# Kernel optimization log

Hardware: AMD Instinct MI355X
Metric: run time of the kernel (lower is better)

Reference implementation:

```python
import jax, jax.numpy as jnp
import numpy as np

N_NODES = 50000
N_EDGES = 1000000
NUM_FEATURES = 32
EDGE_DIM = 16
H = 64
L = 2
BN_EPS = 1e-5
GIN_EPS = 0.0


def _lin(k, fan_in, fan_out, scale=0.1):
    kw, kb = jax.random.split(k)
    W = jax.random.normal(kw, (fan_in, fan_out), jnp.float32) * scale
    b = jax.random.normal(kb, (fan_out,), jnp.float32) * scale
    return W, b


def setup_inputs() -> dict:
    key = jax.random.key(0)
    ks = jax.random.split(key, 12)
    x = jax.random.normal(ks[0], (N_NODES, NUM_FEATURES), jnp.float32)
    edge_index = jax.random.randint(ks[1], (2, N_EDGES), 0, N_NODES, jnp.int64 if jax.config.read('jax_enable_x64') else jnp.int32)
    edge_attr = jax.random.normal(ks[2], (N_EDGES, EDGE_DIM), jnp.float32)
    node_W, node_b = _lin(ks[3], NUM_FEATURES, H)
    edge_W, edge_b = _lin(ks[4], EDGE_DIM, H)

    def stack_lin(k, fan_in, fan_out):
        Ws, bs = zip(*[_lin(kk, fan_in, fan_out) for kk in jax.random.split(k, L)])
        return jnp.stack(Ws), jnp.stack(bs)

    elin_W, elin_b = stack_lin(ks[5], H, H)      # GINEConv internal edge lin
    mlp1_W, mlp1_b = stack_lin(ks[6], H, H)      # GINEConv nn layer 1
    mlp2_W, mlp2_b = stack_lin(ks[7], H, H)      # GINEConv nn layer 2
    emlp1_W, emlp1_b = stack_lin(ks[8], 3 * H, H)  # edge-update MLP layer 1
    emlp2_W, emlp2_b = stack_lin(ks[9], H, H)      # edge-update MLP layer 2
    bn_gamma = jnp.ones((L, H), jnp.float32)
    bn_beta = jnp.zeros((L, H), jnp.float32)
    return dict(x=x, edge_index=edge_index, edge_attr=edge_attr,
                node_W=node_W, node_b=node_b, edge_W=edge_W, edge_b=edge_b,
                elin_W=elin_W, elin_b=elin_b,
                mlp1_W=mlp1_W, mlp1_b=mlp1_b, mlp2_W=mlp2_W, mlp2_b=mlp2_b,
                emlp1_W=emlp1_W, emlp1_b=emlp1_b, emlp2_W=emlp2_W, emlp2_b=emlp2_b,
                bn_gamma=bn_gamma, bn_beta=bn_beta)


def reference(x, edge_index, edge_attr,
              node_W, node_b, edge_W, edge_b,
              elin_W, elin_b, mlp1_W, mlp1_b, mlp2_W, mlp2_b,
              emlp1_W, emlp1_b, emlp2_W, emlp2_b, bn_gamma, bn_beta):
    src, dst = edge_index[0], edge_index[1]
    n = x.shape[0]
    h = x @ node_W + node_b                     # [N, H]
    ea = edge_attr @ edge_W + edge_b            # [E, H]
    for i in range(L):
        # GINEConv: message = relu(x_src + lin(edge_attr)), sum-aggregate at dst
        msg = jax.nn.relu(h[src] + ea @ elin_W[i] + elin_b[i])        # [E, H]
        agg = jax.ops.segment_sum(msg, dst, num_segments=n)           # [N, H]
        out = (1.0 + GIN_EPS) * h + agg
        out = jax.nn.relu(out @ mlp1_W[i] + mlp1_b[i]) @ mlp2_W[i] + mlp2_b[i]
        # BatchNorm (training-mode batch statistics, biased variance)
        mu = out.mean(axis=0)
        var = out.var(axis=0)
        out = (out - mu) * jax.lax.rsqrt(var + BN_EPS) * bn_gamma[i] + bn_beta[i]
        h = (h + jax.nn.relu(out)) * 0.5
        # edge update: gather-concat-MLP residual
        e_in = jnp.concatenate([h[src], h[dst], ea], axis=-1)         # [E, 3H]
        e_up = jax.nn.relu(e_in @ emlp1_W[i] + emlp1_b[i]) @ emlp2_W[i] + emlp2_b[i]
        ea = ea + e_up * 0.5
    return h, ea
```

## Files before the change

### kernel.cpp

```cpp
#include <hip/hip_runtime.h>
#include <hip/hip_bf16.h>

#define NN 50000
#define NE 1000000
#define NF 32
#define ED 16
#define HD 64
#define BN_EPS 1e-5f

typedef unsigned short u16;
typedef __attribute__((ext_vector_type(8))) short bf16x8;
typedef __attribute__((ext_vector_type(4))) float f32x4;

#define WAVE_SYNC() do { \
    asm volatile("s_waitcnt lgkmcnt(0)" ::: "memory"); \
    __builtin_amdgcn_sched_barrier(0); \
} while (0)

__device__ __forceinline__ u16 f2b(float x)
{
    __hip_bfloat16 b = __float2bfloat16(x);
    u16 u; __builtin_memcpy(&u, &b, 2); return u;
}
__device__ __forceinline__ float b2f(u16 u)
{
    uint v = (uint)u << 16; float f; __builtin_memcpy(&f, &v, 4); return f;
}

__global__ __launch_bounds__(256) void k_fill(float* p, float v, size_t n)
{
    size_t i = (size_t)blockIdx.x * 256 + threadIdx.x;
    if (i < n) p[i] = v;
}

__device__ __forceinline__ void gemm4(float (&o)[HD], float4 t, const float* __restrict__ Wr)
{
    #pragma unroll
    for (int f = 0; f < HD; f++) o[f] = fmaf(t.x, Wr[f], o[f]);
    #pragma unroll
    for (int f = 0; f < HD; f++) o[f] = fmaf(t.y, Wr[HD + f], o[f]);
    #pragma unroll
    for (int f = 0; f < HD; f++) o[f] = fmaf(t.z, Wr[2 * HD + f], o[f]);
    #pragma unroll
    for (int f = 0; f < HD; f++) o[f] = fmaf(t.w, Wr[3 * HD + f], o[f]);
}

__global__ __launch_bounds__(256) void k_prep_w1(const float* __restrict__ W, u16* __restrict__ out)
{
    int idx = blockIdx.x * 256 + threadIdx.x;
    if (idx >= 2 * 192 * HD) return;
    int l = idx / (192 * HD), r = idx % (192 * HD), k = r / HD, f = r % HD;
    out[l * 192 * HD + f * 192 + k] = f2b(W[idx]);
}
__global__ __launch_bounds__(256) void k_prep_w64(const float* __restrict__ W, u16* __restrict__ out)
{
    int idx = blockIdx.x * 256 + threadIdx.x;
    if (idx >= 2 * HD * HD) return;
    int l = idx / (HD * HD), r = idx % (HD * HD), k = r / HD, f = r % HD;
    out[l * HD * HD + f * HD + k] = f2b(W[idx]);
}

__global__ __launch_bounds__(256) void k_node_proj(
    const float* __restrict__ x, const float* __restrict__ W,
    const float* __restrict__ b, float* __restrict__ h)
{
    __shared__ float sW[NF * HD];
    for (int t = threadIdx.x; t < NF * HD; t += 256) sW[t] = W[t];
    __syncthreads();
    int lane = threadIdx.x & 63, wv = threadIdx.x >> 6;
    int n = blockIdx.x * 4 + wv;
    if (n >= NN) return;
    float a = (lane < NF) ? x[(size_t)n * NF + lane] : 0.f;
    float acc = b[lane];
    #pragma unroll
    for (int k = 0; k < NF; k++) acc = fmaf(__shfl(a, k), sW[k * HD + lane], acc);
    h[(size_t)n * HD + lane] = acc;
}

__global__ __launch_bounds__(256) void k_edge_proj(
    const float* __restrict__ attr, const float* __restrict__ W,
    const float* __restrict__ b, u16* __restrict__ eab)
{
    size_t e = (size_t)blockIdx.x * 256 + threadIdx.x;
    if (e >= NE) return;
    float o[HD];
    #pragma unroll
    for (int f = 0; f < HD; f++) o[f] = b[f];
    const float4* ar = (const float4*)(attr + e * ED);
    #pragma unroll
    for (int k4 = 0; k4 < ED / 4; k4++)
        gemm4(o, ar[k4], W + (k4 * 4) * HD);
    uint* er = (uint*)(eab + e * HD);
    #pragma unroll
    for (int f2 = 0; f2 < 32; f2++)
        er[f2] = (uint)f2b(o[2 * f2]) | ((uint)f2b(o[2 * f2 + 1]) << 16);
}

__global__ __launch_bounds__(256) void k_gine_msg_mfma(
    const u16* __restrict__ eab, const float* __restrict__ h,
    const int* __restrict__ src, const int* __restrict__ dst,
    const u16* __restrict__ wt, const float* __restrict__ b,
    float* __restrict__ agg)
{
    const int lane = threadIdx.x & 63, wv = threadIdx.x >> 6;
    const size_t base = ((size_t)blockIdx.x * 4 + wv) * 32;
    if (base >= NE) return;
    const int c = lane & 15, g = lane >> 4;

    bf16x8 ae[2][2];
    #pragma unroll
    for (int s = 0; s < 2; s++) {
        const u16* ep = &eab[(base + 16 * s + c) * HD + 8 * g];
        ae[s][0] = *(const bf16x8*)ep;
        ae[s][1] = *(const bf16x8*)(ep + 32);
    }
    int sv[2][4], dv[2][4];
    #pragma unroll
    for (int s = 0; s < 2; s++)
        #pragma unroll
        for (int r = 0; r < 4; r++) {
            sv[s][r] = src[base + 16 * s + 4 * g + r];
            dv[s][r] = dst[base + 16 * s + 4 * g + r];
        }

    f32x4 acc[2][4];
    #pragma unroll
    for (int s = 0; s < 2; s++)
        #pragma unroll
        for (int tt = 0; tt < 4; tt++) {
            float bv = b[tt * 16 + c];
            acc[s][tt] = (f32x4){bv, bv, bv, bv};
        }
    #pragma unroll
    for (int ki = 0; ki < 2; ki++)
        #pragma unroll
        for (int tt = 0; tt < 4; tt++) {
            bf16x8 bw = *(const bf16x8*)&wt[(tt * 16 + c) * HD + ki * 32 + 8 * g];
            acc[0][tt] = __builtin_amdgcn_mfma_f32_16x16x32_bf16(ae[0][ki], bw, acc[0][tt], 0, 0, 0);
            acc[1][tt] = __builtin_amdgcn_mfma_f32_16x16x32_bf16(ae[1][ki], bw, acc[1][tt], 0, 0, 0);
        }
    #pragma unroll
    for (int s = 0; s < 2; s++)
        #pragma unroll
        for (int tt = 0; tt < 4; tt++)
            #pragma unroll
            for (int r = 0; r < 4; r++) {
                float m = acc[s][tt][r] + h[(size_t)sv[s][r] * HD + tt * 16 + c];
                m = fmaxf(m, 0.f);
                unsafeAtomicAdd(&agg[(size_t)dv[s][r] * HD + tt * 16 + c], m);
            }
}

__global__ __launch_bounds__(256) void k_node_mlp(
    const float* __restrict__ h, const float* __restrict__ agg,
    const float* __restrict__ W1, const float* __restrict__ b1,
    const float* __restrict__ W2, const float* __restrict__ b2,
    float* __restrict__ out2)
{
    int n = blockIdx.x * 256 + threadIdx.x;
    if (n >= NN) return;
    float o[HD];
    #pragma unroll
    for (int f = 0; f < HD; f++) o[f] = b1[f];
    const float4* hr = (const float4*)(h + (size_t)n * HD);
    const float4* ar = (const float4*)(agg + (size_t)n * HD);
    #pragma unroll 4
    for (int k4 = 0; k4 < 16; k4++) {
        float4 t1 = hr[k4], t2 = ar[k4];
        float4 t = make_float4(t1.x + t2.x, t1.y + t2.y, t1.z + t2.z, t1.w + t2.w);
        gemm4(o, t, W1 + (k4 * 4) * HD);
    }
    #pragma unroll
    for (int k = 0; k < HD; k++) o[k] = fmaxf(o[k], 0.f);
    #pragma unroll
    for (int c = 0; c < 4; c++) {
        float p[16];
        #pragma unroll
        for (int j = 0; j < 16; j++) p[j] = b2[c * 16 + j];
        for (int k = 0; k < HD; k++) {
            const float* Wr = W2 + k * HD + c * 16;
            #pragma unroll
            for (int j = 0; j < 16; j++) p[j] = fmaf(o[k], Wr[j], p[j]);
        }
        float4* orow = (float4*)(out2 + (size_t)n * HD + c * 16);
        #pragma unroll
        for (int q = 0; q < 4; q++)
            orow[q] = make_float4(p[4*q], p[4*q+1], p[4*q+2], p[4*q+3]);
    }
}

__global__ __launch_bounds__(256) void k_bnstats(
    const float* __restrict__ out2, float* __restrict__ bnst)
{
    int f = threadIdx.x & 63;
    int row0 = blockIdx.x * 4 + (threadIdx.x >> 6);
    float s = 0.f, q = 0.f;
    for (int r = row0; r < NN; r += gridDim.x * 4) {
        float v = out2[(size_t)r * HD + f];
        s += v; q += v * v;
    }
    unsafeAtomicAdd(&bnst[f], s);
    unsafeAtomicAdd(&bnst[HD + f], q);
}

__global__ __launch_bounds__(256) void k_bn_h(
    const float* __restrict__ out2, const float* __restrict__ bnst,
    const float* __restrict__ gamma, const float* __restrict__ beta,
    float* __restrict__ h, u16* __restrict__ hbf, float* __restrict__ hout, int last)
{
    size_t idx = (size_t)blockIdx.x * 256 + threadIdx.x;
    if (idx >= (size_t)NN * HD) return;
    int f = (int)(idx & 63);
    float mu  = bnst[f] * (1.f / NN);
    float var = bnst[HD + f] * (1.f / NN) - mu * mu;
    float sc  = gamma[f] * rsqrtf(var + BN_EPS);
    float sh  = beta[f] - mu * sc;
    float o   = fmaxf(fmaf(out2[idx], sc, sh), 0.f);
    float hn  = (h[idx] + o) * 0.5f;
    h[idx] = hn;
    hbf[idx] = f2b(hn);
    if (last) hout[idx] = hn;
}

__device__ __forceinline__ void edge_mlp_core(
    const u16* __restrict__ hbf, const u16* __restrict__ eab,
    const int* __restrict__ src, const int* __restrict__ dst,
    const u16* __restrict__ w1t, const float* __restrict__ b1,
    const u16* __restrict__ w2t, const float* __restrict__ b2,
    u16* sOw, size_t base, int c, int g, f32x4 (&acc2)[2][4])
{
    int sv[2], dv[2];
    #pragma unroll
    for (int s = 0; s < 2; s++) {
        sv[s] = src[base + 16 * s + c];
        dv[s] = dst[base + 16 * s + c];
    }
    bf16x8 A[3][2][2];
    #pragma unroll
    for (int s = 0; s < 2; s++) {
        const u16* hs = &hbf[(size_t)sv[s] * HD + 8 * g];
        A[0][s][0] = *(const bf16x8*)hs;
        A[0][s][1] = *(const bf16x8*)(hs + 32);
        const u16* hd = &hbf[(size_t)dv[s] * HD + 8 * g];
        A[1][s][0] = *(const bf16x8*)hd;
        A[1][s][1] = *(const bf16x8*)(hd + 32);
        const u16* ep = &eab[(base + 16 * s + c) * HD + 8 * g];
        A[2][s][0] = *(const bf16x8*)ep;
        A[2][s][1] = *(const bf16x8*)(ep + 32);
    }
    f32x4 acc[2][4];
    #pragma unroll
    for (int s = 0; s < 2; s++)
        #pragma unroll
        for (int tt = 0; tt < 4; tt++) {
            float bv = b1[tt * 16 + c];
            acc[s][tt] = (f32x4){bv, bv, bv, bv};
        }
    #pragma unroll
    for (int sec = 0; sec < 3; sec++)
        #pragma unroll
        for (int ki = 0; ki < 2; ki++)
            #pragma unroll
            for (int tt = 0; tt < 4; tt++) {
                bf16x8 bw = *(const bf16x8*)&w1t[(tt * 16 + c) * 192 + sec * 64 + ki * 32 + 8 * g];
                acc[0][tt] = __builtin_amdgcn_mfma_f32_16x16x32_bf16(A[sec][0][ki], bw, acc[0][tt], 0, 0, 0);
                acc[1][tt] = __builtin_amdgcn_mfma_f32_16x16x32_bf16(A[sec][1][ki], bw, acc[1][tt], 0, 0, 0);
            }
    #pragma unroll
    for (int s = 0; s < 2; s++)
        #pragma unroll
        for (int tt = 0; tt < 4; tt++)
            #pragma unroll
            for (int r = 0; r < 4; r++)
                sOw[(16 * s + 4 * g + r) * 72 + tt * 16 + c] = f2b(fmaxf(acc[s][tt][r], 0.f));
    WAVE_SYNC();
    bf16x8 A2[2][2];
    #pragma unroll
    for (int s = 0; s < 2; s++) {
        A2[s][0] = *(const bf16x8*)&sOw[(16 * s + c) * 72 + 8 * g];
        A2[s][1] = *(const bf16x8*)&sOw[(16 * s + c) * 72 + 32 + 8 * g];
    }
    WAVE_SYNC();
    #pragma unroll
    for (int s = 0; s < 2; s++)
        #pragma unroll
        for (int tt = 0; tt < 4; tt++) {
            float bv = b2[tt * 16 + c];
            acc2[s][tt] = (f32x4){bv, bv, bv, bv};
        }
    #pragma unroll
    for (int ki = 0; ki < 2; ki++)
        #pragma unroll
        for (int tt = 0; tt < 4; tt++) {
            bf16x8 bw = *(const bf16x8*)&w2t[(tt * 16 + c) * HD + ki * 32 + 8 * g];
            acc2[0][tt] = __builtin_amdgcn_mfma_f32_16x16x32_bf16(A2[0][ki], bw, acc2[0][tt], 0, 0, 0);
            acc2[1][tt] = __builtin_amdgcn_mfma_f32_16x16x32_bf16(A2[1][ki], bw, acc2[1][tt], 0, 0, 0);
        }
}

__global__ __launch_bounds__(256) void k_edge_upd_fused(
    const u16* __restrict__ hbf, u16* __restrict__ eab,
    const int* __restrict__ src, const int* __restrict__ dst,
    const u16* __restrict__ w1t, const float* __restrict__ b1,
    const u16* __restrict__ w2t, const float* __restrict__ b2,
    const float* __restrict__ h, const u16* __restrict__ welt,
    const float* __restrict__ belin, float* __restrict__ agg)
{
    __shared__ u16 sO[4][32 * 72];
    const int lane = threadIdx.x & 63, wv = threadIdx.x >> 6;
    const size_t base = ((size_t)blockIdx.x * 4 + wv) * 32;
    if (base >= NE) return;
    u16* sOw = sO[wv];
    const int c = lane & 15, g = lane >> 4;

    f32x4 acc2[2][4];
    edge_mlp_core(hbf, eab, src, dst, w1t, b1, w2t, b2, sOw, base, c, g, acc2);

    #pragma unroll
    for (int s = 0; s < 2; s++)
        #pragma unroll
        for (int tt = 0; tt < 4; tt++)
            #pragma unroll
            for (int r = 0; r < 4; r++) {
                size_t a = (base + 16 * s + 4 * g + r) * HD + tt * 16 + c;
                u16 nb = f2b(b2f(eab[a]) + 0.5f * acc2[s][tt][r]);
                eab[a] = nb;
                sOw[(16 * s + 4 * g + r) * 72 + tt * 16 + c] = nb;
            }
    WAVE_SYNC();

    bf16x8 A3[2][2];
    #pragma unroll
    for (int s = 0; s < 2; s++) {
        A3[s][0] = *(const bf16x8*)&sOw[(16 * s + c) * 72 + 8 * g];
        A3[s][1] = *(const bf16x8*)&sOw[(16 * s + c) * 72 + 32 + 8 * g];
    }
    f32x4 acc3[2][4];
    #pragma unroll
    for (int s = 0; s < 2; s++)
        #pragma unroll
        for (int tt = 0; tt < 4; tt++) {
            float bv = belin[tt * 16 + c];
            acc3[s][tt] = (f32x4){bv, bv, bv, bv};
        }
    #pragma unroll
    for (int ki = 0; ki < 2; ki++)
        #pragma unroll
        for (int tt = 0; tt < 4; tt++) {
            bf16x8 bw = *(const bf16x8*)&welt[(tt * 16 + c) * HD + ki * 32 + 8 * g];
            acc3[0][tt] = __builtin_amdgcn_mfma_f32_16x16x32_bf16(A3[0][ki], bw, acc3[0][tt], 0, 0, 0);
            acc3[1][tt] = __builtin_amdgcn_mfma_f32_16x16x32_bf16(A3[1][ki], bw, acc3[1][tt], 0, 0, 0);
        }
    int sv2[2][4], dv2[2][4];
    #pragma unroll
    for (int s = 0; s < 2; s++)
        #pragma unroll
        for (int r = 0; r < 4; r++) {
            sv2[s][r] = src[base + 16 * s + 4 * g + r];
            dv2[s][r] = dst[base + 16 * s + 4 * g + r];
        }
    #pragma unroll
    for (int s = 0; s < 2; s++)
        #pragma unroll
        for (int tt = 0; tt < 4; tt++)
            #pragma unroll
            for (int r = 0; r < 4; r++) {
                float m = acc3[s][tt][r] + h[(size_t)sv2[s][r] * HD + tt * 16 + c];
                m = fmaxf(m, 0.f);
                unsafeAtomicAdd(&agg[(size_t)dv2[s][r] * HD + tt * 16 + c], m);
            }
}

__global__ __launch_bounds__(256) void k_edge_upd_final(
    const u16* __restrict__ hbf, const u16* __restrict__ eab,
    float* __restrict__ eaout,
    const int* __restrict__ src, const int* __restrict__ dst,
    const u16* __restrict__ w1t, const float* __restrict__ b1,
    const u16* __restrict__ w2t, const float* __restrict__ b2)
{
    __shared__ u16 sO[4][32 * 72];
    const int lane = threadIdx.x & 63, wv = threadIdx.x >> 6;
    const size_t base = ((size_t)blockIdx.x * 4 + wv) * 32;
    if (base >= NE) return;
    u16* sOw = sO[wv];
    const int c = lane & 15, g = lane >> 4;

    f32x4 acc2[2][4];
    edge_mlp_core(hbf, eab, src, dst, w1t, b1, w2t, b2, sOw, base, c, g, acc2);

    #pragma unroll
    for (int s = 0; s < 2; s++)
        #pragma unroll
        for (int tt = 0; tt < 4; tt++)
            #pragma unroll
            for (int r = 0; r < 4; r++) {
                size_t a = (base + 16 * s + 4 * g + r) * HD + tt * 16 + c;
                eaout[a] = b2f(eab[a]) + 0.5f * acc2[s][tt][r];
            }
}

extern "C" void kernel_launch(void* const* d_in, const int* in_sizes, int n_in,
                              void* d_out, int out_size, void* d_ws, size_t ws_size,
                              hipStream_t stream)
{
    const float* x        = (const float*)d_in[0];
    const int*   ei       = (const int*)d_in[1];
    const float* eattr    = (const float*)d_in[2];
    const float* node_W   = (const float*)d_in[3];
    const float* node_b   = (const float*)d_in[4];
    const float* edge_W   = (const float*)d_in[5];
    const float* edge_b   = (const float*)d_in[6];
    const float* elin_W   = (const float*)d_in[7];
    const float* elin_b   = (const float*)d_in[8];
    const float* mlp1_W   = (const float*)d_in[9];
    const float* mlp1_b   = (const float*)d_in[10];
    const float* mlp2_W   = (const float*)d_in[11];
    const float* mlp2_b   = (const float*)d_in[12];
    const float* emlp1_W  = (const float*)d_in[13];
    const float* emlp1_b  = (const float*)d_in[14];
    const float* emlp2_W  = (const float*)d_in[15];
    const float* emlp2_b  = (const float*)d_in[16];
    const float* bn_gamma = (const float*)d_in[17];
    const float* bn_beta  = (const float*)d_in[18];

    float* hout = (float*)d_out;
    float* eaout = hout + (size_t)NN * HD;

    const int* src = ei;
    const int* dst = ei + NE;

    float* hbuf = (float*)d_ws;
    float* agg  = hbuf + (size_t)NN * HD;
    float* out2 = agg + (size_t)NN * HD;
    float* bnst = out2 + (size_t)NN * HD;
    u16*   w1t  = (u16*)(bnst + 128);
    u16*   w2t  = w1t + 2 * 192 * HD;
    u16*   welt = w2t + 2 * HD * HD;
    u16*   hbf  = welt + 2 * HD * HD;
    u16*   eab  = hbf + (size_t)NN * HD;
    size_t base_need = ((size_t)NN * HD * 3 + 128) * sizeof(float)
                     + (2 * 192 * HD + 4 * HD * HD + (size_t)NN * HD
                        + (size_t)NE * HD) * sizeof(u16);

    static const int exp_sizes[19] = {
        1600000, 2000000, 16000000, 2048, 64, 1024, 64,
        8192, 128, 8192, 128, 8192, 128, 24576, 128, 8192, 128, 128, 128};
    float sentinel = 0.f;
    if (n_in != 19) sentinel = 6000.f;
    else {
        for (int i = 0; i < 19; i++)
            if (in_sizes[i] != exp_sizes[i]) { sentinel = 2000.f + 32.f * i; break; }
    }
    if (sentinel == 0.f && ws_size < base_need) sentinel = 7000.f;
    if (sentinel != 0.f) {
        k_fill<<<dim3((unsigned)(((size_t)NN * HD + 255) / 256)), dim3(256), 0, stream>>>(
            hout, sentinel, (size_t)NN * HD);
        k_fill<<<dim3((unsigned)(((size_t)NE * HD + 255) / 256)), dim3(256), 0, stream>>>(
            eaout, 0.f, (size_t)NE * HD);
        return;
    }

    dim3 b256(256);
    const unsigned EG  = (NE + 255) / 256;
    const unsigned WG2 = (NE + 127) / 128;
    k_prep_w1<<<dim3((2 * 192 * HD + 255) / 256), b256, 0, stream>>>(emlp1_W, w1t);
    k_prep_w64<<<dim3((2 * HD * HD + 255) / 256), b256, 0, stream>>>(emlp2_W, w2t);
    k_prep_w64<<<dim3((2 * HD * HD + 255) / 256), b256, 0, stream>>>(elin_W, welt);
    k_node_proj<<<dim3((NN + 3) / 4), b256, 0, stream>>>(x, node_W, node_b, hbuf);
    k_edge_proj<<<dim3(EG), b256, 0, stream>>>(eattr, edge_W, edge_b, eab);

    hipMemsetAsync(agg, 0, (size_t)NN * HD * sizeof(float), stream);
    hipMemsetAsync(bnst, 0, 128 * sizeof(float), stream);
    k_gine_msg_mfma<<<dim3(WG2), b256, 0, stream>>>(
        eab, hbuf, src, dst, welt, elin_b, agg);
    k_node_mlp<<<dim3((NN + 255) / 256), b256, 0, stream>>>(
        hbuf, agg, mlp1_W, mlp1_b, mlp2_W, mlp2_b, out2);
    k_bnstats<<<dim3(256), b256, 0, stream>>>(out2, bnst);
    k_bn_h<<<dim3((NN * HD + 255) / 256), b256, 0, stream>>>(
        out2, bnst, bn_gamma, bn_beta, hbuf, hbf, hout, 0);
    hipMemsetAsync(agg, 0, (size_t)NN * HD * sizeof(float), stream);
    hipMemsetAsync(bnst, 0, 128 * sizeof(float), stream);
    k_edge_upd_fused<<<dim3(WG2), b256, 0, stream>>>(
        hbf, eab, src, dst, w1t, emlp1_b, w2t, emlp2_b,
        hbuf, welt + (size_t)HD * HD, elin_b + HD, agg);

    k_node_mlp<<<dim3((NN + 255) / 256), b256, 0, stream>>>(
        hbuf, agg, mlp1_W + HD * HD, mlp1_b + HD,
        mlp2_W + HD * HD, mlp2_b + HD, out2);
    k_bnstats<<<dim3(256), b256, 0, stream>>>(out2, bnst);
    k_bn_h<<<dim3((NN * HD + 255) / 256), b256, 0, stream>>>(
        out2, bnst, bn_gamma + HD, bn_beta + HD, hbuf, hbf, hout, 1);
    k_edge_upd_final<<<dim3(WG2), b256, 0, stream>>>(
        hbf, eab, eaout, src, dst,
        w1t + (size_t)192 * HD, emlp1_b + HD,
        w2t + (size_t)HD * HD, emlp2_b + HD);
}
```

Baseline: 1.063 ms.

## Fuse edge projection into GINE message kernel via MFMA and prefetch gathers

Replaces the scalar per-thread edge projection kernel with an MFMA projection (edge_W zero-padded to K=32 in bf16) fused into the layer-0 GINE message kernel. The projected edge features are written once and reused from LDS for the elin GEMM, so the bf16 edge array is no longer re-read from global memory. In the fused edge update kernels, the src/dst indices, h gathers and old edge values are loaded up front so their latency overlaps the MLP. This raises register pressure, and edge_attr now passes through bf16 before the projection, which lowers its precision.

```diff
diff --git a/kernel.cpp b/kernel.cpp
--- a/kernel.cpp
+++ b/kernel.cpp
@@ -45,6 +45,18 @@
     for (int f = 0; f < HD; f++) o[f] = fmaf(t.w, Wr[3 * HD + f], o[f]);
 }
 
+__device__ __forceinline__ bf16x8 pack8(const float* __restrict__ p)
+{
+    float4 v0 = ((const float4*)p)[0];
+    float4 v1 = ((const float4*)p)[1];
+    union { uint u[4]; bf16x8 v; } r;
+    r.u[0] = (uint)f2b(v0.x) | ((uint)f2b(v0.y) << 16);
+    r.u[1] = (uint)f2b(v0.z) | ((uint)f2b(v0.w) << 16);
+    r.u[2] = (uint)f2b(v1.x) | ((uint)f2b(v1.y) << 16);
+    r.u[3] = (uint)f2b(v1.z) | ((uint)f2b(v1.w) << 16);
+    return r.v;
+}
+
 __global__ __launch_bounds__(256) void k_prep_w1(const float* __restrict__ W, u16* __restrict__ out)
 {
     int idx = blockIdx.x * 256 + threadIdx.x;
@@ -58,6 +70,13 @@
     if (idx >= 2 * HD * HD) return;
     int l = idx / (HD * HD), r = idx % (HD * HD), k = r / HD, f = r % HD;
     out[l * HD * HD + f * HD + k] = f2b(W[idx]);
+}
+__global__ __launch_bounds__(256) void k_prep_wpad(const float* __restrict__ W, u16* __restrict__ out)
+{
+    int idx = blockIdx.x * 256 + threadIdx.x;
+    if (idx >= HD * 32) return;
+    int f = idx / 32, k = idx % 32;
+    out[f * 32 + k] = (k < ED) ? f2b(W[k * HD + f]) : (u16)0;
 }
 
 __global__ __launch_bounds__(256) void k_node_proj(
@@ -77,67 +96,90 @@
     h[(size_t)n * HD + lane] = acc;
 }
 
-__global__ __launch_bounds__(256) void k_edge_proj(
-    const float* __restrict__ attr, const float* __restrict__ W,
-    const float* __restrict__ b, u16* __restrict__ eab)
-{
-    size_t e = (size_t)blockIdx.x * 256 + threadIdx.x;
-    if (e >= NE) return;
-    float o[HD];
-    #pragma unroll
-    for (int f = 0; f < HD; f++) o[f] = b[f];
-    const float4* ar = (const float4*)(attr + e * ED);
-    #pragma unroll
-    for (int k4 = 0; k4 < ED / 4; k4++)
-        gemm4(o, ar[k4], W + (k4 * 4) * HD);
-    uint* er = (uint*)(eab + e * HD);
-    #pragma unroll
-    for (int f2 = 0; f2 < 32; f2++)
-        er[f2] = (uint)f2b(o[2 * f2]) | ((uint)f2b(o[2 * f2 + 1]) << 16);
-}
-
-__global__ __launch_bounds__(256) void k_gine_msg_mfma(
-    const u16* __restrict__ eab, const float* __restrict__ h,
+__global__ __launch_bounds__(256) void k_edge_proj_gine(
+    const float* __restrict__ attr, const float* __restrict__ h,
     const int* __restrict__ src, const int* __restrict__ dst,
-    const u16* __restrict__ wt, const float* __restrict__ b,
-    float* __restrict__ agg)
-{
+    const u16* __restrict__ wpadt, const float* __restrict__ eb,
+    const u16* __restrict__ welt, const float* __restrict__ belin,
+    u16* __restrict__ eab, float* __restrict__ agg)
+{
+    __shared__ u16 sO[4][32 * 72];
     const int lane = threadIdx.x & 63, wv = threadIdx.x >> 6;
     const size_t base = ((size_t)blockIdx.x * 4 + wv) * 32;
     if (base >= NE) return;
+    u16* sOw = sO[wv];
     const int c = lane & 15, g = lane >> 4;
 
-    bf16x8 ae[2][2];
+    int sv2[2][4], dv2[2][4];
+    #pragma unroll
+    for (int s = 0; s < 2; s++)
+        #pragma unroll
+        for (int r = 0; r < 4; r++) {
+            sv2[s][r] = src[base + 16 * s + 4 * g + r];
+            dv2[s][r] = dst[base + 16 * s + 4 * g + r];
+        }
+    float hv[2][4][4];
+    #pragma unroll
+    for (int s = 0; s < 2; s++)
+        #pragma unroll
+        for (int tt = 0; tt < 4; tt++)
+            #pragma unroll
+            for (int r = 0; r < 4; r++)
+                hv[s][tt][r] = h[(size_t)sv2[s][r] * HD + tt * 16 + c];
+
+    bf16x8 zero8 = {0, 0, 0, 0, 0, 0, 0, 0};
+    bf16x8 ap[2];
+    #pragma unroll
+    for (int s = 0; s < 2; s++)
+        ap[s] = (g < 2) ? pack8(attr + (base + 16 * s + c) * ED + 8 * g) : zero8;
+
+    f32x4 acc[2][4];
+    #pragma unroll
+    for (int s = 0; s < 2; s++)
+        #pragma unroll
+        for (int tt = 0; tt < 4; tt++) {
+            float bv = eb[tt * 16 + c];
+            acc[s][tt] = (f32x4){bv, bv, bv, bv};
+        }
+    #pragma unroll
+    for (int tt = 0; tt < 4; tt++) {
+        bf16x8 bw = *(const bf16x8*)&wpadt[(tt * 16 + c) * 32 + 8 * g];
+        acc[0][tt] = __builtin_amdgcn_mfma_f32_16x16x32_bf16(ap[0], bw, acc[0][tt], 0, 0, 0);
+        acc[1][tt] = __builtin_amdgcn_mfma_f32_16x16x32_bf16(ap[1], bw, acc[1][tt], 0, 0, 0);
+    }
+    #pragma unroll
+    for (int s = 0; s < 2; s++)
+        #pragma unroll
+        for (int tt = 0; tt < 4; tt++)
+            #pragma unroll
+            for (int r = 0; r < 4; r++) {
+                u16 nb = f2b(acc[s][tt][r]);
+                eab[(base + 16 * s + 4 * g + r) * HD + tt * 16 + c] = nb;
+                sOw[(16 * s + 4 * g + r) * 72 + tt * 16 + c] = nb;
+            }
+    WAVE_SYNC();
+
+    bf16x8 A3[2][2];
     #pragma unroll
     for (int s = 0; s < 2; s++) {
-        const u16* ep = &eab[(base + 16 * s + c) * HD + 8 * g];
-        ae[s][0] = *(const bf16x8*)ep;
-        ae[s][1] = *(const bf16x8*)(ep + 32);
-    }
-    int sv[2][4], dv[2][4];
-    #pragma unroll
-    for (int s = 0; s < 2; s++)
-        #pragma unroll
-        for (int r = 0; r < 4; r++) {
-            sv[s][r] = src[base + 16 * s + 4 * g + r];
-            dv[s][r] = dst[base + 16 * s + 4 * g + r];
-        }
-
-    f32x4 acc[2][4];
-    #pragma unroll
-    for (int s = 0; s < 2; s++)
-        #pragma unroll
-        for (int tt = 0; tt < 4; tt++) {
-            float bv = b[tt * 16 + c];
-            acc[s][tt] = (f32x4){bv, bv, bv, bv};
+        A3[s][0] = *(const bf16x8*)&sOw[(16 * s + c) * 72 + 8 * g];
+        A3[s][1] = *(const bf16x8*)&sOw[(16 * s + c) * 72 + 32 + 8 * g];
+    }
+    f32x4 acc3[2][4];
+    #pragma unroll
+    for (int s = 0; s < 2; s++)
+        #pragma unroll
+        for (int tt = 0; tt < 4; tt++) {
+            float bv = belin[tt * 16 + c];
+            acc3[s][tt] = (f32x4){bv, bv, bv, bv};
         }
     #pragma unroll
     for (int ki = 0; ki < 2; ki++)
         #pragma unroll
         for (int tt = 0; tt < 4; tt++) {
-            bf16x8 bw = *(const bf16x8*)&wt[(tt * 16 + c) * HD + ki * 32 + 8 * g];
-            acc[0][tt] = __builtin_amdgcn_mfma_f32_16x16x32_bf16(ae[0][ki], bw, acc[0][tt], 0, 0, 0);
-            acc[1][tt] = __builtin_amdgcn_mfma_f32_16x16x32_bf16(ae[1][ki], bw, acc[1][tt], 0, 0, 0);
+            bf16x8 bw = *(const bf16x8*)&welt[(tt * 16 + c) * HD + ki * 32 + 8 * g];
+            acc3[0][tt] = __builtin_amdgcn_mfma_f32_16x16x32_bf16(A3[0][ki], bw, acc3[0][tt], 0, 0, 0);
+            acc3[1][tt] = __builtin_amdgcn_mfma_f32_16x16x32_bf16(A3[1][ki], bw, acc3[1][tt], 0, 0, 0);
         }
     #pragma unroll
     for (int s = 0; s < 2; s++)
@@ -145,9 +187,8 @@
         for (int tt = 0; tt < 4; tt++)
             #pragma unroll
             for (int r = 0; r < 4; r++) {
-                float m = acc[s][tt][r] + h[(size_t)sv[s][r] * HD + tt * 16 + c];
-                m = fmaxf(m, 0.f);
-                unsafeAtomicAdd(&agg[(size_t)dv[s][r] * HD + tt * 16 + c], m);
+                float m = fmaxf(acc3[s][tt][r] + hv[s][tt][r], 0.f);
+                unsafeAtomicAdd(&agg[(size_t)dv2[s][r] * HD + tt * 16 + c], m);
             }
 }
 
@@ -313,6 +354,31 @@
     u16* sOw = sO[wv];
     const int c = lane & 15, g = lane >> 4;
 
+    int sv2[2][4], dv2[2][4];
+    #pragma unroll
+    for (int s = 0; s < 2; s++)
+        #pragma unroll
+        for (int r = 0; r < 4; r++) {
+            sv2[s][r] = src[base + 16 * s + 4 * g + r];
+            dv2[s][r] = dst[base + 16 * s + 4 * g + r];
+        }
+    u16 eold[2][4][4];
+    #pragma unroll
+    for (int s = 0; s < 2; s++)
+        #pragma unroll
+        for (int tt = 0; tt < 4; tt++)
+            #pragma unroll
+            for (int r = 0; r < 4; r++)
+                eold[s][tt][r] = eab[(base + 16 * s + 4 * g + r) * HD + tt * 16 + c];
+    float hv[2][4][4];
+    #pragma unroll
+    for (int s = 0; s < 2; s++)
+        #pragma unroll
+        for (int tt = 0; tt < 4; tt++)
+            #pragma unroll
+            for (int r = 0; r < 4; r++)
+                hv[s][tt][r] = h[(size_t)sv2[s][r] * HD + tt * 16 + c];
+
     f32x4 acc2[2][4];
     edge_mlp_core(hbf, eab, src, dst, w1t, b1, w2t, b2, sOw, base, c, g, acc2);
 
@@ -323,7 +389,7 @@
             #pragma unroll
             for (int r = 0; r < 4; r++) {
                 size_t a = (base + 16 * s + 4 * g + r) * HD + tt * 16 + c;
-                u16 nb = f2b(b2f(eab[a]) + 0.5f * acc2[s][tt][r]);
+                u16 nb = f2b(b2f(eold[s][tt][r]) + 0.5f * acc2[s][tt][r]);
                 eab[a] = nb;
                 sOw[(16 * s + 4 * g + r) * 72 + tt * 16 + c] = nb;
             }
@@ -351,22 +417,13 @@
             acc3[0][tt] = __builtin_amdgcn_mfma_f32_16x16x32_bf16(A3[0][ki], bw, acc3[0][tt], 0, 0, 0);
             acc3[1][tt] = __builtin_amdgcn_mfma_f32_16x16x32_bf16(A3[1][ki], bw, acc3[1][tt], 0, 0, 0);
         }
-    int sv2[2][4], dv2[2][4];
-    #pragma unroll
-    for (int s = 0; s < 2; s++)
-        #pragma unroll
-        for (int r = 0; r < 4; r++) {
-            sv2[s][r] = src[base + 16 * s + 4 * g + r];
-            dv2[s][r] = dst[base + 16 * s + 4 * g + r];
-        }
     #pragma unroll
     for (int s = 0; s < 2; s++)
         #pragma unroll
         for (int tt = 0; tt < 4; tt++)
             #pragma unroll
             for (int r = 0; r < 4; r++) {
-                float m = acc3[s][tt][r] + h[(size_t)sv2[s][r] * HD + tt * 16 + c];
-                m = fmaxf(m, 0.f);
+                float m = fmaxf(acc3[s][tt][r] + hv[s][tt][r], 0.f);
                 unsafeAtomicAdd(&agg[(size_t)dv2[s][r] * HD + tt * 16 + c], m);
             }
 }
@@ -385,6 +442,15 @@
     u16* sOw = sO[wv];
     const int c = lane & 15, g = lane >> 4;
 
+    u16 eold[2][4][4];
+    #pragma unroll
+    for (int s = 0; s < 2; s++)
+        #pragma unroll
+        for (int tt = 0; tt < 4; tt++)
+            #pragma unroll
+            for (int r = 0; r < 4; r++)
+                eold[s][tt][r] = eab[(base + 16 * s + 4 * g + r) * HD + tt * 16 + c];
+
     f32x4 acc2[2][4];
     edge_mlp_core(hbf, eab, src, dst, w1t, b1, w2t, b2, sOw, base, c, g, acc2);
 
@@ -395,7 +461,7 @@
             #pragma unroll
             for (int r = 0; r < 4; r++) {
                 size_t a = (base + 16 * s + 4 * g + r) * HD + tt * 16 + c;
-                eaout[a] = b2f(eab[a]) + 0.5f * acc2[s][tt][r];
+                eaout[a] = b2f(eold[s][tt][r]) + 0.5f * acc2[s][tt][r];
             }
 }
 
@@ -436,10 +502,11 @@
     u16*   w1t  = (u16*)(bnst + 128);
     u16*   w2t  = w1t + 2 * 192 * HD;
     u16*   welt = w2t + 2 * HD * HD;
-    u16*   hbf  = welt + 2 * HD * HD;
+    u16*   wpad = welt + 2 * HD * HD;
+    u16*   hbf  = wpad + HD * 32;
     u16*   eab  = hbf + (size_t)NN * HD;
     size_t base_need = ((size_t)NN * HD * 3 + 128) * sizeof(float)
-                     + (2 * 192 * HD + 4 * HD * HD + (size_t)NN * HD
+                     + (2 * 192 * HD + 4 * HD * HD + HD * 32 + (size_t)NN * HD
                         + (size_t)NE * HD) * sizeof(u16);
 
     static const int exp_sizes[19] = {
@@ -461,18 +528,17 @@
     }
 
     dim3 b256(256);
-    const unsigned EG  = (NE + 255) / 256;
     const unsigned WG2 = (NE + 127) / 128;
     k_prep_w1<<<dim3((2 * 192 * HD + 255) / 256), b256, 0, stream>>>(emlp1_W, w1t);
     k_prep_w64<<<dim3((2 * HD * HD + 255) / 256), b256, 0, stream>>>(emlp2_W, w2t);
     k_prep_w64<<<dim3((2 * HD * HD + 255) / 256), b256, 0, stream>>>(elin_W, welt);
+    k_prep_wpad<<<dim3((HD * 32 + 255) / 256), b256, 0, stream>>>(edge_W, wpad);
     k_node_proj<<<dim3((NN + 3) / 4), b256, 0, stream>>>(x, node_W, node_b, hbuf);
-    k_edge_proj<<<dim3(EG), b256, 0, stream>>>(eattr, edge_W, edge_b, eab);
 
     hipMemsetAsync(agg, 0, (size_t)NN * HD * sizeof(float), stream);
     hipMemsetAsync(bnst, 0, 128 * sizeof(float), stream);
-    k_gine_msg_mfma<<<dim3(WG2), b256, 0, stream>>>(
-        eab, hbuf, src, dst, welt, elin_b, agg);
+    k_edge_proj_gine<<<dim3(WG2), b256, 0, stream>>>(
+        eattr, hbuf, src, dst, wpad, edge_b, welt, elin_b, eab, agg);
     k_node_mlp<<<dim3((NN + 255) / 256), b256, 0, stream>>>(
         hbuf, agg, mlp1_W, mlp1_b, mlp2_W, mlp2_b, out2);
     k_bnstats<<<dim3(256), b256, 0, stream>>>(out2, bnst);
```

New measurement: 1.004 ms. -5.6%, faster.
